# Optimization experiments

Hardware: AMD Instinct MI355X
Metric: run time of the kernel (lower is better)

The kernel has to match this reference:

```python
import jax, jax.numpy as jnp
import numpy as np

N = 50000
E = 800000
IN_C = 128
HID = 16
HEADS = 8
OUT_C = 64
NEG_SLOPE = 0.2


def setup_inputs() -> dict:
    key = jax.random.key(0)
    ks = jax.random.split(key, 12)
    x = jax.random.normal(ks[0], (N, IN_C), dtype=jnp.float32)
    edge_index = jax.random.randint(ks[1], (2, E), 0, N, dtype=jnp.int32)
    s = 0.1
    W1 = jax.random.normal(ks[2], (IN_C, HEADS * HID), dtype=jnp.float32) * s
    a1_src = jax.random.normal(ks[3], (HEADS, HID), dtype=jnp.float32) * s
    a1_dst = jax.random.normal(ks[4], (HEADS, HID), dtype=jnp.float32) * s
    b1 = jnp.zeros((HEADS * HID,), dtype=jnp.float32)
    W2 = jax.random.normal(ks[5], (HEADS * HID, OUT_C), dtype=jnp.float32) * s
    a2_src = jax.random.normal(ks[6], (1, OUT_C), dtype=jnp.float32) * s
    a2_dst = jax.random.normal(ks[7], (1, OUT_C), dtype=jnp.float32) * s
    b2 = jnp.zeros((OUT_C,), dtype=jnp.float32)
    return {"x": x, "edge_index": edge_index, "W1": W1, "a1_src": a1_src,
            "a1_dst": a1_dst, "b1": b1, "W2": W2, "a2_src": a2_src,
            "a2_dst": a2_dst, "b2": b2}


def gat_conv(x, src, dst, W, a_src, a_dst, b, heads, ch):
    # linear projection -> [N, H, C]
    h = (x @ W).reshape(N, heads, ch)
    # per-node attention logits [N, H]
    al_s = jnp.einsum('nhc,hc->nh', h, a_src)
    al_d = jnp.einsum('nhc,hc->nh', h, a_dst)
    # per-edge logits [E, H]
    e = jax.nn.leaky_relu(al_s[src] + al_d[dst], NEG_SLOPE)
    # segment softmax over incoming edges of each dst node
    emax = jax.ops.segment_max(e, dst, num_segments=N)
    ee = jnp.exp(e - emax[dst])
    denom = jax.ops.segment_sum(ee, dst, num_segments=N)
    alpha = ee / (denom[dst] + 1e-16)
    # weighted scatter-aggregate of source messages
    msg = h[src] * alpha[:, :, None]  # [E, H, C]
    out = jax.ops.segment_sum(msg, dst, num_segments=N)
    return out.reshape(N, heads * ch) + b


def reference(x, edge_index, W1, a1_src, a1_dst, b1, W2, a2_src, a2_dst, b2):
    # add self loops (PyG GATConv default add_self_loops=True)
    loops = jnp.arange(N, dtype=edge_index.dtype)
    src = jnp.concatenate([edge_index[0], loops])
    dst = jnp.concatenate([edge_index[1], loops])
    h = gat_conv(x, src, dst, W1, a1_src, a1_dst, b1, HEADS, HID)
    h = jax.nn.relu(h)
    # dropout p=0.6 is identity in eval mode
    out = gat_conv(h, src, dst, W2, a2_src, a2_dst, b2, 1, OUT_C)
    return out
```

## Files before the change

### kernel.cpp

```cpp
#include <hip/hip_runtime.h>
#include <hip/hip_fp16.h>
#include <math.h>

#define N_NODES 50000
#define E_EDGES 800000
#define IN_C    128
#define HID     16
#define HEADS   8
#define OUT_C   64
#define NEG_SLOPE 0.2f
#define CELLW   64

#define WCOLS   144
#define WSTRIDE 136
#define WBYTES  (WCOLS * WSTRIDE * 2)

typedef _Float16 half8 __attribute__((ext_vector_type(8)));
typedef _Float16 half4 __attribute__((ext_vector_type(4)));
typedef float floatx4 __attribute__((ext_vector_type(4)));

__device__ __forceinline__ float lrelu_exp(float v) {
    v = v > 0.f ? v : NEG_SLOPE * v;
    return __expf(v);
}

__device__ __forceinline__ void gload_lds16(const void* g, void* l) {
    __builtin_amdgcn_global_load_lds(
        (const __attribute__((address_space(1))) void*)g,
        (__attribute__((address_space(3))) void*)l, 16, 0, 0);
}

__global__ __launch_bounds__(256) void prep(
    const float* __restrict__ W1, const float* __restrict__ a1_src,
    const float* __restrict__ a1_dst, _Float16* __restrict__ W1t,
    int* __restrict__ cursor) {
    const int t = threadIdx.x;
    const int n = blockIdx.x * 256 + t;
    if (n < N_NODES) cursor[n] = 0;
    if (blockIdx.x == 0) {
        const int col = t & 127;
        const int kq = (t >> 7) * 4;
        for (int it = 0; it < 16; ++it) {
            const int k0 = it * 8 + kq;
            half4 hv;
            hv[0] = (_Float16)W1[(size_t)(k0 + 0) * IN_C + col];
            hv[1] = (_Float16)W1[(size_t)(k0 + 1) * IN_C + col];
            hv[2] = (_Float16)W1[(size_t)(k0 + 2) * IN_C + col];
            hv[3] = (_Float16)W1[(size_t)(k0 + 3) * IN_C + col];
            *(half4*)&W1t[col * WSTRIDE + k0] = hv;
        }
    } else if (blockIdx.x == 1) {
        const int j = t & 15;
        const int k0 = (t >> 4) * 8;
        const float* av = (j < 8) ? (a1_src + j * 16) : (a1_dst + (j - 8) * 16);
        const int hc = (j & 7) * 16;
        for (int k = k0; k < k0 + 8; ++k) {
            float s = 0.f;
#pragma unroll
            for (int c = 0; c < 16; ++c) s += W1[(size_t)k * IN_C + hc + c] * av[c];
            W1t[(128 + j) * WSTRIDE + k] = (_Float16)s;
        }
    }
}

__global__ __launch_bounds__(256) void fused_gemm_fill(
    const float* __restrict__ X, const _Float16* __restrict__ W1t,
    __half* __restrict__ H,
    float* __restrict__ als, float* __restrict__ ald,
    const int* __restrict__ src, const int* __restrict__ dst,
    int* __restrict__ cursor, int* __restrict__ ell) {
    __shared__ _Float16 wT[WCOLS * WSTRIDE];
    const int bid = blockIdx.x;
    const int t = threadIdx.x;

    if (bid & 1) {
        const int tid = (bid >> 1) * 256 + t;
        if (tid < E_EDGES / 4) {
            const int4 s4 = ((const int4*)src)[tid];
            const int4 d4 = ((const int4*)dst)[tid];
            const int p0 = atomicAdd(&cursor[d4.x], 1);
            const int p1 = atomicAdd(&cursor[d4.y], 1);
            const int p2 = atomicAdd(&cursor[d4.z], 1);
            const int p3 = atomicAdd(&cursor[d4.w], 1);
            if (p0 < CELLW) __builtin_nontemporal_store(s4.x, &ell[(size_t)d4.x * CELLW + p0]);
            if (p1 < CELLW) __builtin_nontemporal_store(s4.y, &ell[(size_t)d4.y * CELLW + p1]);
            if (p2 < CELLW) __builtin_nontemporal_store(s4.z, &ell[(size_t)d4.z * CELLW + p2]);
            if (p3 < CELLW) __builtin_nontemporal_store(s4.w, &ell[(size_t)d4.w * CELLW + p3]);
        }
        return;
    }

    {
        const char* g = (const char*)W1t;
        char* l = (char*)wT;
        const int o = t * 16;
#pragma unroll
        for (int it = 0; it < 9; ++it) {
            const int off = it * 4096 + o;
            gload_lds16(g + off, l + off);
        }
        if (t < 144) {
            const int off = 36864 + o;
            gload_lds16(g + off, l + off);
        }
    }

    const int wave = t >> 6, lane = t & 63;
    const int m = lane & 15, quad = lane >> 4;
    const int r0w = (bid >> 1) * 64 + wave * 16;
    int rl = r0w + m;
    if (rl >= N_NODES) rl = N_NODES - 1;
    const float* Xr = X + (size_t)rl * IN_C;

    float4 xv[8];
#pragma unroll
    for (int kc = 0; kc < 4; ++kc) {
        const int k8 = kc * 32 + quad * 8;
        xv[kc * 2]     = *(const float4*)(Xr + k8);
        xv[kc * 2 + 1] = *(const float4*)(Xr + k8 + 4);
    }

    __syncthreads();

    floatx4 acc[9];
#pragma unroll
    for (int i = 0; i < 9; ++i) acc[i] = (floatx4){0.f, 0.f, 0.f, 0.f};

#pragma unroll
    for (int kc = 0; kc < 4; ++kc) {
        const int k8 = kc * 32 + quad * 8;
        const float4 xa = xv[kc * 2];
        const float4 xb = xv[kc * 2 + 1];
        half8 a;
        a[0] = (_Float16)xa.x; a[1] = (_Float16)xa.y;
        a[2] = (_Float16)xa.z; a[3] = (_Float16)xa.w;
        a[4] = (_Float16)xb.x; a[5] = (_Float16)xb.y;
        a[6] = (_Float16)xb.z; a[7] = (_Float16)xb.w;
#pragma unroll
        for (int ct = 0; ct < 9; ++ct) {
            const half8 b = *(const half8*)&wT[(ct * 16 + m) * WSTRIDE + k8];
            acc[ct] = __builtin_amdgcn_mfma_f32_16x16x32_f16(a, b, acc[ct], 0, 0, 0);
        }
    }

    _Float16* Hh = (_Float16*)H;
#pragma unroll
    for (int ct = 0; ct < 8; ++ct) {
#pragma unroll
        for (int r = 0; r < 4; ++r) {
            const int row = r0w + quad * 4 + r;
            if (row < N_NODES)
                Hh[(size_t)row * IN_C + ct * 16 + m] = (_Float16)acc[ct][r];
        }
    }
#pragma unroll
    for (int r = 0; r < 4; ++r) {
        const int row = r0w + quad * 4 + r;
        if (row < N_NODES) {
            if (m < 8) als[(size_t)row * HEADS + m] = acc[8][r];
            else       ald[(size_t)row * HEADS + (m - 8)] = acc[8][r];
        }
    }
}

__global__ __launch_bounds__(256) void agg1_gemm2(
    const int* __restrict__ cnt, const int* __restrict__ ell,
    const float* __restrict__ als, const float* __restrict__ ald,
    const __half* __restrict__ H, const float* __restrict__ b,
    const float* __restrict__ W2, const float* __restrict__ a2_src,
    const float* __restrict__ a2_dst, __half* __restrict__ H2,
    float* __restrict__ als2, float* __restrict__ ald2) {
    __shared__ _Float16 w2T[OUT_C * 136];
    __shared__ _Float16 xrowh[32 * 136];
    __shared__ float l2buf[2][32][2];
    const int t = threadIdx.x;

    {
        const int col = t & 63;
        const int kg = t >> 6;
        for (int k0 = kg * 32; k0 < kg * 32 + 32; k0 += 4) {
            half4 hv;
            hv[0] = (_Float16)W2[(size_t)(k0 + 0) * OUT_C + col];
            hv[1] = (_Float16)W2[(size_t)(k0 + 1) * OUT_C + col];
            hv[2] = (_Float16)W2[(size_t)(k0 + 2) * OUT_C + col];
            hv[3] = (_Float16)W2[(size_t)(k0 + 3) * OUT_C + col];
            *(half4*)&w2T[col * 136 + k0] = hv;
        }
    }

    const int nl = t >> 3, h = t & 7;
    int nc = blockIdx.x * 32 + nl;
    if (nc >= N_NODES) nc = N_NODES - 1;
    int deg = cnt[nc];
    deg = deg < CELLW ? deg : CELLW;
    const int* ep = ell + (size_t)nc * CELLW;
    const float ad = ald[nc * HEADS + h];
    float accv[16];
    float ssum;
    {
        const float w = lrelu_exp(als[nc * HEADS + h] + ad);
        const half8* q = (const half8*)(H + ((size_t)nc * HEADS + h) * HID);
        const half8 u0 = q[0], u1 = q[1];
        ssum = w;
#pragma unroll
        for (int j = 0; j < 8; ++j) {
            accv[j] = w * (float)u0[j];
            accv[j + 8] = w * (float)u1[j];
        }
    }
    for (int p = 0; p < deg; p += 4) {
        const int4 s4 = *(const int4*)(ep + p);
        const int s0 = s4.x;
        const int i1 = (p + 1 < deg) ? s4.y : nc;
        const int i2 = (p + 2 < deg) ? s4.z : nc;
        const int i3 = (p + 3 < deg) ? s4.w : nc;
        const float f1 = (p + 1 < deg) ? 1.f : 0.f;
        const float f2 = (p + 2 < deg) ? 1.f : 0.f;
        const float f3 = (p + 3 < deg) ? 1.f : 0.f;
        const float v0 = als[s0 * HEADS + h];
        const float v1 = als[i1 * HEADS + h];
        const float v2 = als[i2 * HEADS + h];
        const float v3 = als[i3 * HEADS + h];
        const half8* q0 = (const half8*)(H + ((size_t)s0 * HEADS + h) * HID);
        const half8* q1 = (const half8*)(H + ((size_t)i1 * HEADS + h) * HID);
        const half8* q2 = (const half8*)(H + ((size_t)i2 * HEADS + h) * HID);
        const half8* q3 = (const half8*)(H + ((size_t)i3 * HEADS + h) * HID);
        const half8 a0 = q0[0], b0 = q0[1];
        const half8 a1 = q1[0], b1 = q1[1];
        const half8 a2 = q2[0], b2 = q2[1];
        const half8 a3 = q3[0], b3 = q3[1];
        const float w0 = lrelu_exp(v0 + ad);
        const float w1 = lrelu_exp(v1 + ad) * f1;
        const float w2 = lrelu_exp(v2 + ad) * f2;
        const float w3 = lrelu_exp(v3 + ad) * f3;
        ssum += (w0 + w1) + (w2 + w3);
#pragma unroll
        for (int j = 0; j < 8; ++j) {
            accv[j]     += w0 * (float)a0[j] + w1 * (float)a1[j] +
                           w2 * (float)a2[j] + w3 * (float)a3[j];
            accv[j + 8] += w0 * (float)b0[j] + w1 * (float)b1[j] +
                           w2 * (float)b2[j] + w3 * (float)b3[j];
        }
    }
    {
        const float inv = 1.f / (ssum + 1e-16f);
        half8 r0, r1;
#pragma unroll
        for (int j = 0; j < 8; ++j) {
            float ra = accv[j] * inv + b[h * 16 + j];
            float rb = accv[j + 8] * inv + b[h * 16 + 8 + j];
            r0[j] = (_Float16)(ra > 0.f ? ra : 0.f);
            r1[j] = (_Float16)(rb > 0.f ? rb : 0.f);
        }
        _Float16* xr = &xrowh[nl * 136 + h * 16];
        *(half8*)(xr) = r0;
        *(half8*)(xr + 8) = r1;
    }

    __syncthreads();

    {
        const int wv = t >> 6, ln = t & 63;
        const int bm = ln & 15, quad = ln >> 4;
        const int mt = wv >> 1;
        const int ntg = wv & 1;
        floatx4 acc0 = (floatx4){0.f, 0.f, 0.f, 0.f};
        floatx4 acc1 = (floatx4){0.f, 0.f, 0.f, 0.f};
        const _Float16* arow  = &xrowh[(mt * 16 + bm) * 136];
        const _Float16* brow0 = &w2T[(ntg * 32 + bm) * 136];
        const _Float16* brow1 = &w2T[(ntg * 32 + 16 + bm) * 136];
#pragma unroll
        for (int kc = 0; kc < 4; ++kc) {
            const int k8 = kc * 32 + quad * 8;
            const half8 a   = *(const half8*)(arow + k8);
            const half8 b0v = *(const half8*)(brow0 + k8);
            const half8 b1v = *(const half8*)(brow1 + k8);
            acc0 = __builtin_amdgcn_mfma_f32_16x16x32_f16(a, b0v, acc0, 0, 0, 0);
            acc1 = __builtin_amdgcn_mfma_f32_16x16x32_f16(a, b1v, acc1, 0, 0, 0);
        }
        const float a2s0 = a2_src[ntg * 32 + bm],      a2d0 = a2_dst[ntg * 32 + bm];
        const float a2s1 = a2_src[ntg * 32 + 16 + bm], a2d1 = a2_dst[ntg * 32 + 16 + bm];
        _Float16* H2h = (_Float16*)H2;
        float psr[4], pdr[4];
#pragma unroll
        for (int r = 0; r < 4; ++r) {
            const float c0 = acc0[r], c1 = acc1[r];
            float ps = c0 * a2s0 + c1 * a2s1;
            float pd = c0 * a2d0 + c1 * a2d1;
            ps += __shfl_xor(ps, 1); pd += __shfl_xor(pd, 1);
            ps += __shfl_xor(ps, 2); pd += __shfl_xor(pd, 2);
            ps += __shfl_xor(ps, 4); pd += __shfl_xor(pd, 4);
            ps += __shfl_xor(ps, 8); pd += __shfl_xor(pd, 8);
            psr[r] = ps; pdr[r] = pd;
            const int row = blockIdx.x * 32 + mt * 16 + quad * 4 + r;
            if (row < N_NODES) {
                H2h[(size_t)row * OUT_C + ntg * 32 + bm] = (_Float16)c0;
                H2h[(size_t)row * OUT_C + ntg * 32 + 16 + bm] = (_Float16)c1;
            }
        }
        if (bm == 0) {
#pragma unroll
            for (int r = 0; r < 4; ++r) {
                l2buf[ntg][mt * 16 + quad * 4 + r][0] = psr[r];
                l2buf[ntg][mt * 16 + quad * 4 + r][1] = pdr[r];
            }
        }
    }
    __syncthreads();
    if (t < 32) {
        const int n2 = blockIdx.x * 32 + t;
        if (n2 < N_NODES) {
            als2[n2] = l2buf[0][t][0] + l2buf[1][t][0];
            ald2[n2] = l2buf[0][t][1] + l2buf[1][t][1];
        }
    }
}

__global__ __launch_bounds__(256) void agg2(
    const int* __restrict__ cnt, const int* __restrict__ ell,
    const float* __restrict__ als, const float* __restrict__ ald,
    const __half* __restrict__ H, const float* __restrict__ b,
    float* __restrict__ out) {
    const int t = threadIdx.x;
    int n = blockIdx.x * 32 + (t >> 3);
    const int j0 = (t & 7) * 8;
    const bool valid = n < N_NODES;
    if (!valid) n = N_NODES - 1;
    int deg = cnt[n];
    deg = deg < CELLW ? deg : CELLW;
    const int* ep = ell + (size_t)n * CELLW;
    const float ad = ald[n];
    float accv[8];
    float ssum;
    {
        const float w = lrelu_exp(als[n] + ad);
        const half8 u = *(const half8*)(H + (size_t)n * OUT_C + j0);
        ssum = w;
#pragma unroll
        for (int k = 0; k < 8; ++k) accv[k] = w * (float)u[k];
    }
    for (int p = 0; p < deg; p += 4) {
        const int4 s4 = *(const int4*)(ep + p);
        const int s0 = s4.x;
        const int i1 = (p + 1 < deg) ? s4.y : n;
        const int i2 = (p + 2 < deg) ? s4.z : n;
        const int i3 = (p + 3 < deg) ? s4.w : n;
        const float f1 = (p + 1 < deg) ? 1.f : 0.f;
        const float f2 = (p + 2 < deg) ? 1.f : 0.f;
        const float f3 = (p + 3 < deg) ? 1.f : 0.f;
        const float v0 = als[s0];
        const float v1 = als[i1];
        const float v2 = als[i2];
        const float v3 = als[i3];
        const half8 u0 = *(const half8*)(H + (size_t)s0 * OUT_C + j0);
        const half8 u1 = *(const half8*)(H + (size_t)i1 * OUT_C + j0);
        const half8 u2 = *(const half8*)(H + (size_t)i2 * OUT_C + j0);
        const half8 u3 = *(const half8*)(H + (size_t)i3 * OUT_C + j0);
        const float w0 = lrelu_exp(v0 + ad);
        const float w1 = lrelu_exp(v1 + ad) * f1;
        const float w2 = lrelu_exp(v2 + ad) * f2;
        const float w3 = lrelu_exp(v3 + ad) * f3;
        ssum += (w0 + w1) + (w2 + w3);
#pragma unroll
        for (int k = 0; k < 8; ++k)
            accv[k] += w0 * (float)u0[k] + w1 * (float)u1[k] +
                       w2 * (float)u2[k] + w3 * (float)u3[k];
    }
    if (valid) {
        const float inv = 1.f / (ssum + 1e-16f);
        floatx4 r0, r1;
        r0[0] = accv[0] * inv + b[j0 + 0]; r0[1] = accv[1] * inv + b[j0 + 1];
        r0[2] = accv[2] * inv + b[j0 + 2]; r0[3] = accv[3] * inv + b[j0 + 3];
        r1[0] = accv[4] * inv + b[j0 + 4]; r1[1] = accv[5] * inv + b[j0 + 5];
        r1[2] = accv[6] * inv + b[j0 + 6]; r1[3] = accv[7] * inv + b[j0 + 7];
        float* op = out + (size_t)n * OUT_C + j0;
        __builtin_nontemporal_store(r0, (floatx4*)op);
        __builtin_nontemporal_store(r1, (floatx4*)(op + 4));
    }
}

extern "C" void kernel_launch(void* const* d_in, const int* in_sizes, int n_in,
                              void* d_out, int out_size, void* d_ws, size_t ws_size,
                              hipStream_t stream) {
    const float* x      = (const float*)d_in[0];
    const int*   ei     = (const int*)d_in[1];
    const float* W1     = (const float*)d_in[2];
    const float* a1_src = (const float*)d_in[3];
    const float* a1_dst = (const float*)d_in[4];
    const float* b1     = (const float*)d_in[5];
    const float* W2     = (const float*)d_in[6];
    const float* a2_src = (const float*)d_in[7];
    const float* a2_dst = (const float*)d_in[8];
    const float* b2     = (const float*)d_in[9];
    const int* src = ei;
    const int* dst = ei + E_EDGES;
    float* outp = (float*)d_out;

    char* wsb = (char*)d_ws;
    __half* h1   = (__half*)wsb;
    __half* h2   = h1 + (size_t)N_NODES * IN_C;
    float*  als1 = (float*)(h2 + (size_t)N_NODES * OUT_C);
    float*  ald1 = als1 + N_NODES * HEADS;
    float*  als2 = ald1 + N_NODES * HEADS;
    float*  ald2 = als2 + N_NODES;
    int*    cursor = (int*)(ald2 + N_NODES);
    int*    ell    = cursor + N_NODES;

    _Float16* W1t = (_Float16*)als2;

    prep<<<(N_NODES + 255) / 256, 256, 0, stream>>>(W1, a1_src, a1_dst, W1t, cursor);

    {
        const int gemm_blocks = (N_NODES + 63) / 64;
        fused_gemm_fill<<<gemm_blocks * 2, 256, 0, stream>>>(
            x, W1t, h1, als1, ald1, src, dst, cursor, ell);
    }

    agg1_gemm2<<<(N_NODES + 31) / 32, 256, 0, stream>>>(
        cursor, ell, als1, ald1, h1, b1, W2, a2_src, a2_dst, h2, als2, ald2);

    agg2<<<(N_NODES + 31) / 32, 256, 0, stream>>>(
        cursor, ell, als2, ald2, h2, b2, outp);
}
```

Measured before the change: 190.7 us.

## Split edge lists across thread pairs and precompute W2 transpose in prep

```diff
diff --git a/kernel.cpp b/kernel.cpp
--- a/kernel.cpp
+++ b/kernel.cpp
@@ -32,7 +32,8 @@
 
 __global__ __launch_bounds__(256) void prep(
     const float* __restrict__ W1, const float* __restrict__ a1_src,
-    const float* __restrict__ a1_dst, _Float16* __restrict__ W1t,
+    const float* __restrict__ a1_dst, const float* __restrict__ W2,
+    _Float16* __restrict__ W1t, _Float16* __restrict__ W2t,
     int* __restrict__ cursor) {
     const int t = threadIdx.x;
     const int n = blockIdx.x * 256 + t;
@@ -60,6 +61,17 @@
             for (int c = 0; c < 16; ++c) s += W1[(size_t)k * IN_C + hc + c] * av[c];
             W1t[(128 + j) * WSTRIDE + k] = (_Float16)s;
         }
+    } else if (blockIdx.x == 2) {
+        const int col = t & 63;
+        const int kg = t >> 6;
+        for (int k0 = kg * 32; k0 < kg * 32 + 32; k0 += 4) {
+            half4 hv;
+            hv[0] = (_Float16)W2[(size_t)(k0 + 0) * OUT_C + col];
+            hv[1] = (_Float16)W2[(size_t)(k0 + 1) * OUT_C + col];
+            hv[2] = (_Float16)W2[(size_t)(k0 + 2) * OUT_C + col];
+            hv[3] = (_Float16)W2[(size_t)(k0 + 3) * OUT_C + col];
+            *(half4*)&W2t[col * 136 + k0] = hv;
+        }
     }
 }
 
@@ -167,37 +179,24 @@
     const int* __restrict__ cnt, const int* __restrict__ ell,
     const float* __restrict__ als, const float* __restrict__ ald,
     const __half* __restrict__ H, const float* __restrict__ b,
-    const float* __restrict__ W2, const float* __restrict__ a2_src,
+    const _Float16* __restrict__ W2t, const float* __restrict__ a2_src,
     const float* __restrict__ a2_dst, __half* __restrict__ H2,
     float* __restrict__ als2, float* __restrict__ ald2) {
-    __shared__ _Float16 w2T[OUT_C * 136];
-    __shared__ _Float16 xrowh[32 * 136];
-    __shared__ float l2buf[2][32][2];
+    __shared__ _Float16 xrowh[16 * 136];
+    __shared__ float l2buf[4][16][2];
     const int t = threadIdx.x;
 
-    {
-        const int col = t & 63;
-        const int kg = t >> 6;
-        for (int k0 = kg * 32; k0 < kg * 32 + 32; k0 += 4) {
-            half4 hv;
-            hv[0] = (_Float16)W2[(size_t)(k0 + 0) * OUT_C + col];
-            hv[1] = (_Float16)W2[(size_t)(k0 + 1) * OUT_C + col];
-            hv[2] = (_Float16)W2[(size_t)(k0 + 2) * OUT_C + col];
-            hv[3] = (_Float16)W2[(size_t)(k0 + 3) * OUT_C + col];
-            *(half4*)&w2T[col * 136 + k0] = hv;
-        }
-    }
-
-    const int nl = t >> 3, h = t & 7;
-    int nc = blockIdx.x * 32 + nl;
-    if (nc >= N_NODES) nc = N_NODES - 1;
+    const int nl = t >> 4;
+    const int h  = (t >> 1) & 7;
+    const int e2 = t & 1;
+    const int nc = blockIdx.x * 16 + nl;
     int deg = cnt[nc];
     deg = deg < CELLW ? deg : CELLW;
     const int* ep = ell + (size_t)nc * CELLW;
     const float ad = ald[nc * HEADS + h];
     float accv[16];
     float ssum;
-    {
+    if (e2 == 0) {
         const float w = lrelu_exp(als[nc * HEADS + h] + ad);
         const half8* q = (const half8*)(H + ((size_t)nc * HEADS + h) * HID);
         const half8 u0 = q[0], u1 = q[1];
@@ -207,8 +206,12 @@
             accv[j] = w * (float)u0[j];
             accv[j + 8] = w * (float)u1[j];
         }
-    }
-    for (int p = 0; p < deg; p += 4) {
+    } else {
+        ssum = 0.f;
+#pragma unroll
+        for (int j = 0; j < 16; ++j) accv[j] = 0.f;
+    }
+    for (int p = 4 * e2; p < deg; p += 8) {
         const int4 s4 = *(const int4*)(ep + p);
         const int s0 = s4.x;
         const int i1 = (p + 1 < deg) ? s4.y : nc;
@@ -242,7 +245,11 @@
                            w2 * (float)b2[j] + w3 * (float)b3[j];
         }
     }
-    {
+    ssum += __shfl_xor(ssum, 1);
+#pragma unroll
+    for (int j = 0; j < 16; ++j) accv[j] += __shfl_xor(accv[j], 1);
+
+    if (e2 == 0) {
         const float inv = 1.f / (ssum + 1e-16f);
         half8 r0, r1;
 #pragma unroll
@@ -262,57 +269,44 @@
     {
         const int wv = t >> 6, ln = t & 63;
         const int bm = ln & 15, quad = ln >> 4;
-        const int mt = wv >> 1;
-        const int ntg = wv & 1;
-        floatx4 acc0 = (floatx4){0.f, 0.f, 0.f, 0.f};
-        floatx4 acc1 = (floatx4){0.f, 0.f, 0.f, 0.f};
-        const _Float16* arow  = &xrowh[(mt * 16 + bm) * 136];
-        const _Float16* brow0 = &w2T[(ntg * 32 + bm) * 136];
-        const _Float16* brow1 = &w2T[(ntg * 32 + 16 + bm) * 136];
+        floatx4 acc = (floatx4){0.f, 0.f, 0.f, 0.f};
+        const _Float16* arow = &xrowh[bm * 136];
+        const _Float16* brow = &W2t[(wv * 16 + bm) * 136];
 #pragma unroll
         for (int kc = 0; kc < 4; ++kc) {
             const int k8 = kc * 32 + quad * 8;
-            const half8 a   = *(const half8*)(arow + k8);
-            const half8 b0v = *(const half8*)(brow0 + k8);
-            const half8 b1v = *(const half8*)(brow1 + k8);
-            acc0 = __builtin_amdgcn_mfma_f32_16x16x32_f16(a, b0v, acc0, 0, 0, 0);
-            acc1 = __builtin_amdgcn_mfma_f32_16x16x32_f16(a, b1v, acc1, 0, 0, 0);
-        }
-        const float a2s0 = a2_src[ntg * 32 + bm],      a2d0 = a2_dst[ntg * 32 + bm];
-        const float a2s1 = a2_src[ntg * 32 + 16 + bm], a2d1 = a2_dst[ntg * 32 + 16 + bm];
+            const half8 a  = *(const half8*)(arow + k8);
+            const half8 bv = *(const half8*)(brow + k8);
+            acc = __builtin_amdgcn_mfma_f32_16x16x32_f16(a, bv, acc, 0, 0, 0);
+        }
+        const float a2s = a2_src[wv * 16 + bm], a2d = a2_dst[wv * 16 + bm];
         _Float16* H2h = (_Float16*)H2;
         float psr[4], pdr[4];
 #pragma unroll
         for (int r = 0; r < 4; ++r) {
-            const float c0 = acc0[r], c1 = acc1[r];
-            float ps = c0 * a2s0 + c1 * a2s1;
-            float pd = c0 * a2d0 + c1 * a2d1;
+            const float c = acc[r];
+            float ps = c * a2s, pd = c * a2d;
             ps += __shfl_xor(ps, 1); pd += __shfl_xor(pd, 1);
             ps += __shfl_xor(ps, 2); pd += __shfl_xor(pd, 2);
             ps += __shfl_xor(ps, 4); pd += __shfl_xor(pd, 4);
             ps += __shfl_xor(ps, 8); pd += __shfl_xor(pd, 8);
             psr[r] = ps; pdr[r] = pd;
-            const int row = blockIdx.x * 32 + mt * 16 + quad * 4 + r;
-            if (row < N_NODES) {
-                H2h[(size_t)row * OUT_C + ntg * 32 + bm] = (_Float16)c0;
-                H2h[(size_t)row * OUT_C + ntg * 32 + 16 + bm] = (_Float16)c1;
+            const int row = blockIdx.x * 16 + quad * 4 + r;
+            H2h[(size_t)row * OUT_C + wv * 16 + bm] = (_Float16)c;
+        }
+        if (bm == 0) {
+#pragma unroll
+            for (int r = 0; r < 4; ++r) {
+                l2buf[wv][quad * 4 + r][0] = psr[r];
+                l2buf[wv][quad * 4 + r][1] = pdr[r];
             }
         }
-        if (bm == 0) {
-#pragma unroll
-            for (int r = 0; r < 4; ++r) {
-                l2buf[ntg][mt * 16 + quad * 4 + r][0] = psr[r];
-                l2buf[ntg][mt * 16 + quad * 4 + r][1] = pdr[r];
-            }
-        }
     }
     __syncthreads();
-    if (t < 32) {
-        const int n2 = blockIdx.x * 32 + t;
-        if (n2 < N_NODES) {
-            als2[n2] = l2buf[0][t][0] + l2buf[1][t][0];
-            ald2[n2] = l2buf[0][t][1] + l2buf[1][t][1];
-        }
+    if (t < 16) {
+        const int n2 = blockIdx.x * 16 + t;
+        als2[n2] = (l2buf[0][t][0] + l2buf[1][t][0]) + (l2buf[2][t][0] + l2buf[3][t][0]);
+        ald2[n2] = (l2buf[0][t][1] + l2buf[1][t][1]) + (l2buf[2][t][1] + l2buf[3][t][1]);
     }
 }
 
@@ -322,24 +316,29 @@
     const __half* __restrict__ H, const float* __restrict__ b,
     float* __restrict__ out) {
     const int t = threadIdx.x;
-    int n = blockIdx.x * 32 + (t >> 3);
-    const int j0 = (t & 7) * 8;
-    const bool valid = n < N_NODES;
-    if (!valid) n = N_NODES - 1;
+    const int nl = t >> 4;
+    const int jc = (t >> 1) & 7;
+    const int e2 = t & 1;
+    const int n = blockIdx.x * 16 + nl;
+    const int j0 = jc * 8;
     int deg = cnt[n];
     deg = deg < CELLW ? deg : CELLW;
     const int* ep = ell + (size_t)n * CELLW;
     const float ad = ald[n];
     float accv[8];
     float ssum;
-    {
+    if (e2 == 0) {
         const float w = lrelu_exp(als[n] + ad);
         const half8 u = *(const half8*)(H + (size_t)n * OUT_C + j0);
         ssum = w;
 #pragma unroll
         for (int k = 0; k < 8; ++k) accv[k] = w * (float)u[k];
-    }
-    for (int p = 0; p < deg; p += 4) {
+    } else {
+        ssum = 0.f;
+#pragma unroll
+        for (int k = 0; k < 8; ++k) accv[k] = 0.f;
+    }
+    for (int p = 4 * e2; p < deg; p += 8) {
         const int4 s4 = *(const int4*)(ep + p);
         const int s0 = s4.x;
         const int i1 = (p + 1 < deg) ? s4.y : n;
@@ -366,7 +365,11 @@
             accv[k] += w0 * (float)u0[k] + w1 * (float)u1[k] +
                        w2 * (float)u2[k] + w3 * (float)u3[k];
     }
-    if (valid) {
+    ssum += __shfl_xor(ssum, 1);
+#pragma unroll
+    for (int k = 0; k < 8; ++k) accv[k] += __shfl_xor(accv[k], 1);
+
+    if (e2 == 0) {
         const float inv = 1.f / (ssum + 1e-16f);
         floatx4 r0, r1;
         r0[0] = accv[0] * inv + b[j0 + 0]; r0[1] = accv[1] * inv + b[j0 + 1];
@@ -405,10 +408,11 @@
     float*  ald2 = als2 + N_NODES;
     int*    cursor = (int*)(ald2 + N_NODES);
     int*    ell    = cursor + N_NODES;
+    _Float16* W2t  = (_Float16*)(ell + (size_t)N_NODES * CELLW);
 
     _Float16* W1t = (_Float16*)als2;
 
-    prep<<<(N_NODES + 255) / 256, 256, 0, stream>>>(W1, a1_src, a1_dst, W1t, cursor);
+    prep<<<(N_NODES + 255) / 256, 256, 0, stream>>>(W1, a1_src, a1_dst, W2, W1t, W2t, cursor);
 
     {
         const int gemm_blocks = (N_NODES + 63) / 64;
@@ -416,9 +420,9 @@
             x, W1t, h1, als1, ald1, src, dst, cursor, ell);
     }
 
-    agg1_gemm2<<<(N_NODES + 31) / 32, 256, 0, stream>>>(
-        cursor, ell, als1, ald1, h1, b1, W2, a2_src, a2_dst, h2, als2, ald2);
-
-    agg2<<<(N_NODES + 31) / 32, 256, 0, stream>>>(
+    agg1_gemm2<<<N_NODES / 16, 256, 0, stream>>>(
+        cursor, ell, als1, ald1, h1, b1, W2t, a2_src, a2_dst, h2, als2, ald2);
+
+    agg2<<<N_NODES / 16, 256, 0, stream>>>(
         cursor, ell, als2, ald2, h2, b2, outp);
 }
```

New measurement: 190.4 us. No clear change (-0.1%).
